# Performance work log

Hardware: AMD Instinct MI355X
Metric: run time of the kernel (lower is better)

The kernel has to match this reference:

```python
import jax, jax.numpy as jnp
import numpy as np

N, IN, H, C = 100000, 128, 4, 64  # nodes, in_channels, heads, out_channels
E0 = 1600000
NEG_SLOPE = 0.2


def setup_inputs() -> dict:
    key = jax.random.key(0)
    ks = jax.random.split(key, 8)
    x = jax.random.normal(ks[0], (N, IN), dtype=jnp.float32)
    edge_index = jax.random.randint(ks[1], (2, E0), 0, N, dtype=jnp.int64)
    s = 1.0 / np.sqrt(IN)
    W = jax.random.uniform(ks[2], (IN, H * C), jnp.float32, -s, s)
    att_src = jax.random.normal(ks[3], (H, C), jnp.float32) * 0.1
    att_dst = jax.random.normal(ks[4], (H, C), jnp.float32) * 0.1
    bias = jnp.zeros((C,), jnp.float32)
    sf = 1.0 / np.sqrt(C)
    fc_w = jax.random.uniform(ks[5], (C, 1), jnp.float32, -sf, sf)
    fc_b = jax.random.uniform(ks[6], (1,), jnp.float32, -sf, sf)
    return {"x": x, "edge_index": edge_index, "W": W, "att_src": att_src,
            "att_dst": att_dst, "bias": bias, "fc_w": fc_w, "fc_b": fc_b}


def gat_forward(x, edge_index, W, att_src, att_dst, bias, fc_w, fc_b):
    n = x.shape[0]
    # add self-loops (PyG GATConv default)
    loops = jnp.arange(n, dtype=edge_index.dtype)
    src = jnp.concatenate([edge_index[0], loops])
    dst = jnp.concatenate([edge_index[1], loops])

    h = (x @ W).reshape(n, H, C)                     # [N,H,C]
    a_src = jnp.einsum('nhc,hc->nh', h, att_src)     # [N,H]
    a_dst = jnp.einsum('nhc,hc->nh', h, att_dst)

    logits = jax.nn.leaky_relu(a_src[src] + a_dst[dst], NEG_SLOPE)  # [E,H]
    m = jax.ops.segment_max(logits, dst, num_segments=n)            # [N,H]
    e = jnp.exp(logits - m[dst])
    z = jax.ops.segment_sum(e, dst, num_segments=n)                 # [N,H]
    alpha = e / (z[dst] + 1e-16)                                    # [E,H]

    msgs = h[src] * alpha[:, :, None]                               # [E,H,C]
    out = jax.ops.segment_sum(msgs, dst, num_segments=n)            # [N,H,C]
    out = out.mean(axis=1) + bias                                   # concat=False -> head mean

    out = jax.nn.relu(out)
    return jax.nn.sigmoid(out @ fc_w + fc_b)                        # [N,1]


def reference(x, edge_index, W, att_src, att_dst, bias, fc_w, fc_b):
    return gat_forward(x, edge_index, W, att_src, att_dst, bias, fc_w, fc_b)
```

## Files before the change

kernel.cpp:

```cpp
#include <hip/hip_runtime.h>


#define NN 100000
#define IN_DIM 128
#define HC 256
#define NEG_SLOPE 0.2f
#define NB 1563
#define HB 128

typedef __attribute__((ext_vector_type(8))) __bf16 bf16x8;
typedef __attribute__((ext_vector_type(4))) float f32x4;
typedef __attribute__((ext_vector_type(2))) float f32x2;

__global__ __launch_bounds__(256, 4) void k_gemm(const float* __restrict__ x,
    const float* __restrict__ W, const float* __restrict__ att_src,
    const float* __restrict__ att_dst, unsigned char* __restrict__ h8,
    float* __restrict__ a_src, float* __restrict__ a_dst, int n_tiles) {
  const int tid = threadIdx.x;
  const int cg = blockIdx.x & 3;
  const int rblk = blockIdx.x >> 2;
  const int wave = tid >> 6, lane = tid & 63;
  const int g = lane >> 4, i16 = lane & 15;

  bf16x8 wf[4][4];
  float as_l[4], ad_l[4];
  #pragma unroll
  for (int nt = 0; nt < 4; ++nt) {
    const int col = cg * 64 + nt * 16 + i16;
    as_l[nt] = att_src[col];
    ad_l[nt] = att_dst[col];
    #pragma unroll
    for (int kk = 0; kk < 4; ++kk) {
      const float* wp = W + (size_t)(kk * 32 + g * 8) * HC + col;
      bf16x8 f;
      #pragma unroll
      for (int j = 0; j < 8; ++j) f[j] = (__bf16)wp[(size_t)j * HC];
      wf[nt][kk] = f;
    }
  }

  for (int t = rblk; t < n_tiles; t += 256) {
    const int rbase = t * 64 + wave * 16;
    int arow = rbase + i16; if (arow >= NN) arow = NN - 1;
    const float* xp = x + (size_t)arow * IN_DIM;
    f32x4 acc[4];
    #pragma unroll
    for (int nt = 0; nt < 4; ++nt) acc[nt] = (f32x4){0.f, 0.f, 0.f, 0.f};
    #pragma unroll
    for (int kk = 0; kk < 4; ++kk) {
      const int k0 = kk * 32 + g * 8;
      f32x4 xa = *(const f32x4*)(xp + k0);
      f32x4 xb = *(const f32x4*)(xp + k0 + 4);
      bf16x8 af;
      af[0] = (__bf16)xa[0]; af[1] = (__bf16)xa[1];
      af[2] = (__bf16)xa[2]; af[3] = (__bf16)xa[3];
      af[4] = (__bf16)xb[0]; af[5] = (__bf16)xb[1];
      af[6] = (__bf16)xb[2]; af[7] = (__bf16)xb[3];
      #pragma unroll
      for (int nt = 0; nt < 4; ++nt)
        acc[nt] = __builtin_amdgcn_mfma_f32_16x16x32_bf16(af, wf[nt][kk], acc[nt], 0, 0, 0);
    }
    float ps[4] = {0.f, 0.f, 0.f, 0.f}, pd[4] = {0.f, 0.f, 0.f, 0.f};
    #pragma unroll
    for (int nt = 0; nt < 4; ++nt) {
      #pragma unroll
      for (int r = 0; r < 4; ++r) {
        ps[r] += acc[nt][r] * as_l[nt];
        pd[r] += acc[nt][r] * ad_l[nt];
      }
    }
    #pragma unroll
    for (int r = 0; r < 4; ++r) {
      #pragma unroll
      for (int d = 1; d <= 8; d <<= 1) {
        ps[r] += __shfl_xor(ps[r], d);
        pd[r] += __shfl_xor(pd[r], d);
      }
      const int row = rbase + g * 4 + r;
      if (row < NN) {
        if (i16 == 0) {
          a_src[(size_t)row * 4 + cg] = ps[r];
          a_dst[(size_t)row * 4 + cg] = pd[r];
        }
        unsigned char* hp = h8 + (size_t)row * HC + cg * 64 + i16;
        #pragma unroll
        for (int nt = 0; nt < 4; ++nt) {
          unsigned int pv = __builtin_amdgcn_cvt_pk_fp8_f32(acc[nt][r], acc[nt][r], 0, false);
          hp[nt * 16] = (unsigned char)pv;
        }
      }
    }
  }
}

__global__ __launch_bounds__(256) void k_hist(const int* __restrict__ ei,
    int* __restrict__ bh, int e0, int ch) {
  __shared__ int h[NB];
  const int b = blockIdx.x, tid = threadIdx.x;
  for (int k = tid; k < NB; k += 256) h[k] = 0;
  __syncthreads();
  const int lo = b * ch, hi = min(lo + ch, e0);
  for (int e = lo + tid; e < hi; e += 256)
    atomicAdd(&h[((unsigned)ei[e0 + e]) >> 6], 1);
  __syncthreads();
  for (int k = tid; k < NB; k += 256) bh[(size_t)b * NB + k] = h[k];
}

__global__ __launch_bounds__(256) void k_colscan(int* __restrict__ bh,
                                                 int* __restrict__ total) {
  int k = blockIdx.x * 256 + threadIdx.x;
  if (k >= NB) return;
  int run = 0;
  for (int b = 0; b < HB; ++b) {
    size_t i = (size_t)b * NB + k;
    int t = bh[i]; bh[i] = run; run += t;
  }
  total[k] = run;
}

__global__ __launch_bounds__(256) void k_bscan(const int* __restrict__ total,
                                               int* __restrict__ base, int e0) {
  __shared__ int ls[256];
  const int t = threadIdx.x;
  int vals[7]; int lsum = 0;
  #pragma unroll
  for (int i = 0; i < 7; ++i) {
    int k = t * 7 + i;
    vals[i] = (k < NB) ? total[k] : 0;
    lsum += vals[i];
  }
  ls[t] = lsum; __syncthreads();
  for (int off = 1; off < 256; off <<= 1) {
    int v = (t >= off) ? ls[t - off] : 0;
    __syncthreads(); ls[t] += v; __syncthreads();
  }
  int excl = (t == 0) ? 0 : ls[t - 1];
  #pragma unroll
  for (int i = 0; i < 7; ++i) {
    int k = t * 7 + i;
    if (k < NB) base[k] = excl;
    excl += vals[i];
  }
  if (t == 255) base[NB] = e0;
}

__global__ __launch_bounds__(256) void k_scat(const int* __restrict__ ei,
    const int* __restrict__ bh, const int* __restrict__ base,
    uint2* __restrict__ rec, int e0, int ch) {
  __shared__ int cur[NB];
  const int b = blockIdx.x, tid = threadIdx.x;
  for (int k = tid; k < NB; k += 256)
    cur[k] = base[k] + bh[(size_t)b * NB + k];
  __syncthreads();
  const int lo = b * ch, hi = min(lo + ch, e0);
  for (int e = lo + tid; e < hi; e += 256) {
    int s = ei[e], d = ei[e0 + e];
    int p = atomicAdd(&cur[((unsigned)d) >> 6], 1);
    rec[p] = (uint2){(unsigned)d, (unsigned)s};
  }
}

__global__ __launch_bounds__(256) void k_bsort(const uint2* __restrict__ rec,
    const int* __restrict__ base, int* __restrict__ csr,
    int* __restrict__ rowptr, int e0) {
  __shared__ int cnt64[64], pre[64];
  const int k = blockIdx.x, tid = threadIdx.x;
  const int lo = base[k], hi = base[k + 1];
  if (tid < 64) cnt64[tid] = 0;
  __syncthreads();
  for (int i = lo + tid; i < hi; i += 256)
    atomicAdd(&cnt64[rec[i].x & 63], 1);
  __syncthreads();
  if (tid == 0) {
    int run = 0;
    for (int j = 0; j < 64; ++j) { pre[j] = run; run += cnt64[j]; }
  }
  __syncthreads();
  if (tid < 64) {
    int n = k * 64 + tid;
    if (n < NN) rowptr[n] = lo + pre[tid];
    cnt64[tid] = lo + pre[tid];
  }
  if (k == NB - 1 && tid == 0) rowptr[NN] = e0;
  __syncthreads();
  for (int i = lo + tid; i < hi; i += 256) {
    uint2 r = rec[i];
    int p = atomicAdd(&cnt64[r.x & 63], 1);
    csr[p] = (int)r.y;
  }
}

__global__ __launch_bounds__(256) void k_main(const unsigned char* __restrict__ h8,
    const float* __restrict__ a_src, const float* __restrict__ a_dst,
    const int* __restrict__ rowptr, const int* __restrict__ csr,
    const float* __restrict__ bias, const float* __restrict__ fc_w,
    const float* __restrict__ fc_b, float* __restrict__ out, int n0) {
  const int tid = threadIdx.x, lane = tid & 63;
  const int n = n0 + blockIdx.x * 4 + (tid >> 6);
  if (n >= NN) return;
  const int eh = lane >> 5;
  const int c8 = lane & 31;
  const int head = c8 >> 3;
  const float wz = ((c8 & 7) == 0) ? 1.f : 0.f;
  const unsigned char* __restrict__ hb = h8 + c8 * 8;
  const float adh = a_dst[n * 4 + head];
  const int beg = rowptr[n];
  const int end = rowptr[n + 1];
  const int ne = end - beg;

  float a0, a1, a2, a3, a4, a5, a6, a7, zl;
  {
    float lg = a_src[n * 4 + head] + adh;
    lg = fmaxf(lg, NEG_SLOPE * lg);
    const float ev = (eh == 0) ? __expf(lg) : 0.f;
    zl = wz * ev;
    const uint2 hv = *(const uint2*)(hb + ((size_t)n << 8));
    const f32x2 f01 = __builtin_amdgcn_cvt_pk_f32_fp8(hv.x, false);
    const f32x2 f23 = __builtin_amdgcn_cvt_pk_f32_fp8(hv.x, true);
    const f32x2 f45 = __builtin_amdgcn_cvt_pk_f32_fp8(hv.y, false);
    const f32x2 f67 = __builtin_amdgcn_cvt_pk_f32_fp8(hv.y, true);
    a0 = ev * f01[0]; a1 = ev * f01[1];
    a2 = ev * f23[0]; a3 = ev * f23[1];
    a4 = ev * f45[0]; a5 = ev * f45[1];
    a6 = ev * f67[0]; a7 = ev * f67[1];
  }

  int b0 = beg;
  const int bend = beg + (ne & ~7);
  for (; b0 < bend; b0 += 8) {
    #pragma unroll
    for (int u = 0; u < 4; ++u) {
      const int sv = csr[b0 + u * 2 + eh];
      float lg = a_src[sv * 4 + head] + adh;
      lg = fmaxf(lg, NEG_SLOPE * lg);
      const float ev = __expf(lg);
      zl += wz * ev;
      const uint2 hv = *(const uint2*)(hb + ((size_t)sv << 8));
      const f32x2 f01 = __builtin_amdgcn_cvt_pk_f32_fp8(hv.x, false);
      const f32x2 f23 = __builtin_amdgcn_cvt_pk_f32_fp8(hv.x, true);
      const f32x2 f45 = __builtin_amdgcn_cvt_pk_f32_fp8(hv.y, false);
      const f32x2 f67 = __builtin_amdgcn_cvt_pk_f32_fp8(hv.y, true);
      a0 += ev * f01[0]; a1 += ev * f01[1];
      a2 += ev * f23[0]; a3 += ev * f23[1];
      a4 += ev * f45[0]; a5 += ev * f45[1];
      a6 += ev * f67[0]; a7 += ev * f67[1];
    }
  }
  for (; b0 < end; b0 += 2) {
    const int idx = b0 + eh;
    const bool v = idx < end;
    const int sv = csr[v ? idx : beg];
    float lg = a_src[sv * 4 + head] + adh;
    lg = fmaxf(lg, NEG_SLOPE * lg);
    float ev = v ? __expf(lg) : 0.f;
    zl += wz * ev;
    const uint2 hv = *(const uint2*)(hb + ((size_t)sv << 8));
    const f32x2 f01 = __builtin_amdgcn_cvt_pk_f32_fp8(hv.x, false);
    const f32x2 f23 = __builtin_amdgcn_cvt_pk_f32_fp8(hv.x, true);
    const f32x2 f45 = __builtin_amdgcn_cvt_pk_f32_fp8(hv.y, false);
    const f32x2 f67 = __builtin_amdgcn_cvt_pk_f32_fp8(hv.y, true);
    a0 += ev * f01[0]; a1 += ev * f01[1];
    a2 += ev * f23[0]; a3 += ev * f23[1];
    a4 += ev * f45[0]; a5 += ev * f45[1];
    a6 += ev * f67[0]; a7 += ev * f67[1];
  }
  a0 += __shfl_xor(a0, 32); a1 += __shfl_xor(a1, 32);
  a2 += __shfl_xor(a2, 32); a3 += __shfl_xor(a3, 32);
  a4 += __shfl_xor(a4, 32); a5 += __shfl_xor(a5, 32);
  a6 += __shfl_xor(a6, 32); a7 += __shfl_xor(a7, 32);
  zl += __shfl_xor(zl, 32);
  zl += __shfl_xor(zl, 1); zl += __shfl_xor(zl, 2); zl += __shfl_xor(zl, 4);
  const float rz = 0.25f / (zl + 1e-16f);
  a0 *= rz; a1 *= rz; a2 *= rz; a3 *= rz;
  a4 *= rz; a5 *= rz; a6 *= rz; a7 *= rz;
  a0 += __shfl_xor(a0, 8); a0 += __shfl_xor(a0, 16);
  a1 += __shfl_xor(a1, 8); a1 += __shfl_xor(a1, 16);
  a2 += __shfl_xor(a2, 8); a2 += __shfl_xor(a2, 16);
  a3 += __shfl_xor(a3, 8); a3 += __shfl_xor(a3, 16);
  a4 += __shfl_xor(a4, 8); a4 += __shfl_xor(a4, 16);
  a5 += __shfl_xor(a5, 8); a5 += __shfl_xor(a5, 16);
  a6 += __shfl_xor(a6, 8); a6 += __shfl_xor(a6, 16);
  a7 += __shfl_xor(a7, 8); a7 += __shfl_xor(a7, 16);

  const int ch0 = (c8 & 7) * 8;
  const f32x4 bv0 = *(const f32x4*)(bias + ch0);
  const f32x4 bv1 = *(const f32x4*)(bias + ch0 + 4);
  const f32x4 wv0 = *(const f32x4*)(fc_w + ch0);
  const f32x4 wv1 = *(const f32x4*)(fc_w + ch0 + 4);
  float p = fmaxf(a0 + bv0[0], 0.f) * wv0[0] + fmaxf(a1 + bv0[1], 0.f) * wv0[1]
          + fmaxf(a2 + bv0[2], 0.f) * wv0[2] + fmaxf(a3 + bv0[3], 0.f) * wv0[3]
          + fmaxf(a4 + bv1[0], 0.f) * wv1[0] + fmaxf(a5 + bv1[1], 0.f) * wv1[1]
          + fmaxf(a6 + bv1[2], 0.f) * wv1[2] + fmaxf(a7 + bv1[3], 0.f) * wv1[3];
  p += __shfl_xor(p, 1); p += __shfl_xor(p, 2); p += __shfl_xor(p, 4);
  if (lane == 0) out[n] = 1.f / (1.f + __expf(-(p + fc_b[0])));
}

extern "C" void kernel_launch(void* const* d_in, const int* in_sizes, int n_in,
                              void* d_out, int out_size, void* d_ws, size_t ws_size,
                              hipStream_t stream) {
  const float* x       = (const float*)d_in[0];
  const int*   ei      = (const int*)d_in[1];
  const float* W       = (const float*)d_in[2];
  const float* att_src = (const float*)d_in[3];
  const float* att_dst = (const float*)d_in[4];
  const float* bias    = (const float*)d_in[5];
  const float* fc_w    = (const float*)d_in[6];
  const float* fc_b    = (const float*)d_in[7];
  float* out = (float*)d_out;
  const int e0 = in_sizes[1] / 2;

  char* ws = (char*)d_ws;
  size_t off = 0;
  auto carve = [&](size_t bytes) {
    void* p = ws + off;
    off = (off + bytes + 255) & ~(size_t)255;
    return p;
  };
  unsigned char* h8 = (unsigned char*)carve((size_t)NN * HC);
  float* a_src = (float*)carve((size_t)NN * 4 * 4);
  float* a_dst = (float*)carve((size_t)NN * 4 * 4);
  int* bh      = (int*)carve((size_t)HB * NB * 4);
  int* total   = (int*)carve((size_t)NB * 4);
  int* base    = (int*)carve((size_t)(NB + 1) * 4);
  int* rowptr  = (int*)carve((size_t)(NN + 1) * 4);
  uint2* rec   = (uint2*)carve((size_t)e0 * 8);
  int* csrbuf  = (int*)carve((size_t)e0 * 4);

  const int n_tiles = (NN + 63) / 64;
  const int ch = (e0 + HB - 1) / HB;
  k_gemm<<<dim3(1024), dim3(256), 0, stream>>>(x, W, att_src, att_dst,
                                               h8, a_src, a_dst, n_tiles);
  k_hist<<<dim3(HB), dim3(256), 0, stream>>>(ei, bh, e0, ch);
  k_colscan<<<dim3((NB + 255) / 256), dim3(256), 0, stream>>>(bh, total);
  k_bscan<<<dim3(1), dim3(256), 0, stream>>>(total, base, e0);
  k_scat<<<dim3(HB), dim3(256), 0, stream>>>(ei, bh, base, rec, e0, ch);
  k_bsort<<<dim3(NB), dim3(256), 0, stream>>>(rec, base, csrbuf, rowptr, e0);
  const int third = 8334;
  k_main<<<dim3(third), dim3(256), 0, stream>>>(h8, a_src, a_dst, rowptr, csrbuf,
                                                bias, fc_w, fc_b, out, 0);
  k_main<<<dim3(third), dim3(256), 0, stream>>>(h8, a_src, a_dst, rowptr, csrbuf,
                                                bias, fc_w, fc_b, out, 33336);
  k_main<<<dim3(8333), dim3(256), 0, stream>>>(h8, a_src, a_dst, rowptr, csrbuf,
                                               bias, fc_w, fc_b, out, 66672);
}
```

Baseline: 322.4 us.

## Widen histogram/scatter grid, parallelize column scan per wave, double GEMM grid

Raises the number of histogram/scatter blocks from 128 to 512 so the edge bucketing uses more CUs. It rewrites the column scan so each wave scans one bucket column across 512 blocks with a shuffle-based prefix sum, replacing one serial thread per column. It also doubles the GEMM grid and remaps block indices so each group of 8 row-blocks shares a column group. The cost is a larger per-block histogram buffer and more scan traffic.

New measurement: 306.7 us. 4.9% less time.

```diff
diff --git a/kernel.cpp b/kernel.cpp
--- a/kernel.cpp
+++ b/kernel.cpp
@@ -6,7 +6,7 @@
 #define HC 256
 #define NEG_SLOPE 0.2f
 #define NB 1563
-#define HB 128
+#define HB 512
 
 typedef __attribute__((ext_vector_type(8))) __bf16 bf16x8;
 typedef __attribute__((ext_vector_type(4))) float f32x4;
@@ -17,8 +17,9 @@
     const float* __restrict__ att_dst, unsigned char* __restrict__ h8,
     float* __restrict__ a_src, float* __restrict__ a_dst, int n_tiles) {
   const int tid = threadIdx.x;
-  const int cg = blockIdx.x & 3;
-  const int rblk = blockIdx.x >> 2;
+  const int bid = blockIdx.x;
+  const int cg = (bid >> 3) & 3;
+  const int rblk = (bid & 7) | ((bid >> 5) << 3);
   const int wave = tid >> 6, lane = tid & 63;
   const int g = lane >> 4, i16 = lane & 15;
 
@@ -39,7 +40,7 @@
     }
   }
 
-  for (int t = rblk; t < n_tiles; t += 256) {
+  for (int t = rblk; t < n_tiles; t += 512) {
     const int rbase = t * 64 + wave * 16;
     int arow = rbase + i16; if (arow >= NN) arow = NN - 1;
     const float* xp = x + (size_t)arow * IN_DIM;
@@ -108,14 +109,29 @@
 
 __global__ __launch_bounds__(256) void k_colscan(int* __restrict__ bh,
                                                  int* __restrict__ total) {
-  int k = blockIdx.x * 256 + threadIdx.x;
-  if (k >= NB) return;
-  int run = 0;
-  for (int b = 0; b < HB; ++b) {
-    size_t i = (size_t)b * NB + k;
-    int t = bh[i]; bh[i] = run; run += t;
-  }
-  total[k] = run;
+  const int wv = blockIdx.x * 4 + (threadIdx.x >> 6);
+  if (wv >= NB) return;
+  const int lane = threadIdx.x & 63;
+  int v[8]; int s = 0;
+  #pragma unroll
+  for (int i = 0; i < 8; ++i) {
+    v[i] = bh[(size_t)(lane * 8 + i) * NB + wv];
+    s += v[i];
+  }
+  int run = s;
+  #pragma unroll
+  for (int d = 1; d < 64; d <<= 1) {
+    int t = __shfl_up(run, d);
+    if (lane >= d) run += t;
+  }
+  int acc = run - s;
+  #pragma unroll
+  for (int i = 0; i < 8; ++i) {
+    int t = v[i];
+    bh[(size_t)(lane * 8 + i) * NB + wv] = acc;
+    acc += t;
+  }
+  if (lane == 63) total[wv] = acc;
 }
 
 __global__ __launch_bounds__(256) void k_bscan(const int* __restrict__ total,
@@ -328,10 +344,10 @@
 
   const int n_tiles = (NN + 63) / 64;
   const int ch = (e0 + HB - 1) / HB;
-  k_gemm<<<dim3(1024), dim3(256), 0, stream>>>(x, W, att_src, att_dst,
+  k_gemm<<<dim3(2048), dim3(256), 0, stream>>>(x, W, att_src, att_dst,
                                                h8, a_src, a_dst, n_tiles);
   k_hist<<<dim3(HB), dim3(256), 0, stream>>>(ei, bh, e0, ch);
-  k_colscan<<<dim3((NB + 255) / 256), dim3(256), 0, stream>>>(bh, total);
+  k_colscan<<<dim3((NB + 3) / 4), dim3(256), 0, stream>>>(bh, total);
   k_bscan<<<dim3(1), dim3(256), 0, stream>>>(total, base, e0);
   k_scat<<<dim3(HB), dim3(256), 0, stream>>>(ei, bh, base, rec, e0, ch);
   k_bsort<<<dim3(NB), dim3(256), 0, stream>>>(rec, base, csrbuf, rowptr, e0);
```
